# Performance work log

Hardware: AMD Instinct MI355X
Metric: run time of the kernel (lower is better)

Reference implementation:

```python
import jax, jax.numpy as jnp
import numpy as np

N_NODES = 50000
N_EDGES = 640000
IN_FEATS = 512
HID = 128
OUT_FEATS = 128
N_GRAPHS = 256


def setup_inputs() -> dict:
    key = jax.random.key(0)
    ks = jax.random.split(key, 7)
    x = jax.random.normal(ks[0], (N_NODES, IN_FEATS), dtype=jnp.float32)
    edge_index = jax.random.randint(ks[1], (2, N_EDGES), 0, N_NODES, dtype=jnp.int32)
    batch = jnp.sort(jax.random.randint(ks[2], (N_NODES,), 0, N_GRAPHS, dtype=jnp.int32))
    W1 = jax.random.normal(ks[3], (IN_FEATS, HID), dtype=jnp.float32) * (1.0 / np.sqrt(IN_FEATS))
    b1 = jnp.zeros((HID,), jnp.float32)
    W2 = jax.random.normal(ks[4], (HID, OUT_FEATS), dtype=jnp.float32) * (1.0 / np.sqrt(HID))
    b2 = jnp.zeros((OUT_FEATS,), jnp.float32)
    return {"x": x, "W1": W1, "b1": b1, "W2": W2, "b2": b2,
            "edge_index": edge_index, "batch": batch}


def reference(x, W1, b1, W2, b2, edge_index, batch):
    N = x.shape[0]
    loop = jnp.arange(N, dtype=edge_index.dtype)
    # PyG GCNConv default: add self-loops, symmetric deg^-1/2 normalization
    row = jnp.concatenate([edge_index[0], loop])  # source
    col = jnp.concatenate([edge_index[1], loop])  # target
    deg = jax.ops.segment_sum(jnp.ones_like(col, x.dtype), col, num_segments=N)
    dinv = jnp.where(deg > 0, jax.lax.rsqrt(deg), 0.0)
    norm = dinv[row] * dinv[col]  # [E+N]

    def gcn_conv(h, W, b):
        h = h @ W  # linear transform first (PyG order)
        msg = h[row] * norm[:, None]  # gather + scale
        agg = jax.ops.segment_sum(msg, col, num_segments=N)  # scatter-add
        return agg + b

    h = jax.nn.relu(gcn_conv(x, W1, b1))  # dropout is identity in eval mode
    h = gcn_conv(h, W2, b2)
    hs = jax.ops.segment_sum(h, batch, num_segments=N_GRAPHS)  # global_add_pool
    return hs, h
```

## Files before the change

kernel.cpp:

```cpp
#include <hip/hip_runtime.h>
#include <hip/hip_bf16.h>

#define N_NODES  50000
#define N_EDGES  640000
#define IN_FEATS 512
#define HID      128
#define OUT_FEATS 128
#define N_GRAPHS 256

#define SCAN_CHUNK 1024
#define SCAN_BLOCKS ((N_NODES + SCAN_CHUNK - 1) / SCAN_CHUNK)

typedef __attribute__((ext_vector_type(8))) short short8;
typedef __attribute__((ext_vector_type(4))) float f32x4;

__device__ __forceinline__ float bf2f(unsigned u16) {
    return __uint_as_float(u16 << 16);
}
__device__ __forceinline__ unsigned short f2bf(float f) {
    __hip_bfloat16 h = __float2bfloat16(f);
    return *(unsigned short*)&h;
}


#define PREP_BLOCKS 840

__global__ __launch_bounds__(256) void k_prep(const float* __restrict__ W1,
                                              const float* __restrict__ W2,
                                              const int* __restrict__ batch,
                                              unsigned short* __restrict__ wt1,
                                              unsigned short* __restrict__ wt2,
                                              int* __restrict__ cnt,
                                              int* __restrict__ gstart,
                                              float* __restrict__ hs) {
    int b = blockIdx.x;
    int t = threadIdx.x;
    if (b < 196) {
        int i = b * 256 + t;
        if (i < N_NODES) {
            int bt = batch[i];
            int bp = (i == 0) ? -1 : batch[i - 1];
            for (int g = bp + 1; g <= bt; ++g) gstart[g] = i;
            if (i == N_NODES - 1)
                for (int g = bt + 1; g <= N_GRAPHS; ++g) gstart[g] = N_NODES;
        }
    } else if (b < 392) {
        int i = (b - 196) * 256 + t;
        if (i < N_NODES) cnt[i] = 0;
    } else if (b < 648) {
        int idx = (b - 392) * 256 + t;
        int n = idx & 127, k = idx >> 7;
        wt1[(size_t)n * IN_FEATS + k] = f2bf(W1[(size_t)k * 128 + n]);
    } else if (b < 712) {
        int idx = (b - 648) * 256 + t;
        int n = idx & 127, k = idx >> 7;
        wt2[(size_t)n * HID + k] = f2bf(W2[(size_t)k * 128 + n]);
    } else {
        int idx = (b - 712) * 256 + t;
        hs[idx] = 0.f;
    }
}


__global__ void k_count(const int* __restrict__ col, int* __restrict__ cnt) {
    int e = blockIdx.x * blockDim.x + threadIdx.x;
    if (e < N_EDGES) atomicAdd(&cnt[col[e]], 1);
}

__global__ __launch_bounds__(256) void k_scan_a(const int* __restrict__ cnt,
                                                int* __restrict__ offs,
                                                int* __restrict__ bsum) {
    __shared__ int sums[256];
    int t = threadIdx.x;
    int base = blockIdx.x * SCAN_CHUNK + t * 4;
    int c0 = 0, c1 = 0, c2 = 0, c3 = 0;
    if (base + 3 < N_NODES) {
        int4 v = *(const int4*)(cnt + base);
        c0 = v.x; c1 = v.y; c2 = v.z; c3 = v.w;
    } else {
        if (base + 0 < N_NODES) c0 = cnt[base + 0];
        if (base + 1 < N_NODES) c1 = cnt[base + 1];
        if (base + 2 < N_NODES) c2 = cnt[base + 2];
    }
    int ts = c0 + c1 + c2 + c3;
    sums[t] = ts;
    __syncthreads();
#pragma unroll
    for (int off = 1; off < 256; off <<= 1) {
        int add = (t >= off) ? sums[t - off] : 0;
        __syncthreads();
        sums[t] += add;
        __syncthreads();
    }
    int ex = sums[t] - ts;
    if (base + 3 < N_NODES) {
        int4 o;
        o.x = ex; o.y = ex + c0; o.z = ex + c0 + c1; o.w = ex + c0 + c1 + c2;
        *(int4*)(offs + base) = o;
    } else {
        if (base + 0 < N_NODES) offs[base + 0] = ex;
        if (base + 1 < N_NODES) offs[base + 1] = ex + c0;
        if (base + 2 < N_NODES) offs[base + 2] = ex + c0 + c1;
    }
    if (t == 255) bsum[blockIdx.x] = sums[255];
}

__global__ __launch_bounds__(256) void k_scan_c(const int* __restrict__ cnt,
                                                const int* __restrict__ bsum,
                                                int* __restrict__ offs,
                                                int* __restrict__ cursor,
                                                float* __restrict__ dinv) {
    __shared__ int sb[64];
    int t = threadIdx.x;
    int b = blockIdx.x;
    if (t < 64) sb[t] = (t < SCAN_BLOCKS) ? bsum[t] : 0;
    __syncthreads();
#pragma unroll
    for (int off = 1; off < 64; off <<= 1) {
        int add = 0;
        if (t < 64 && t >= off) add = sb[t - off];
        __syncthreads();
        if (t < 64) sb[t] += add;
        __syncthreads();
    }
    int add = (b == 0) ? 0 : sb[b - 1];
    int base = b * SCAN_CHUNK + t * 4;
    if (base + 3 < N_NODES) {
        int4 o = *(const int4*)(offs + base);
        o.x += add; o.y += add; o.z += add; o.w += add;
        *(int4*)(offs + base) = o;
        *(int4*)(cursor + base) = o;
        int4 c = *(const int4*)(cnt + base);
        float4 d;
        d.x = rsqrtf((float)c.x + 1.0f);
        d.y = rsqrtf((float)c.y + 1.0f);
        d.z = rsqrtf((float)c.z + 1.0f);
        d.w = rsqrtf((float)c.w + 1.0f);
        *(float4*)(dinv + base) = d;
    } else {
#pragma unroll
        for (int j = 0; j < 4; ++j) {
            int i = base + j;
            if (i < N_NODES) {
                int o = offs[i] + add;
                offs[i] = o; cursor[i] = o;
                dinv[i] = rsqrtf((float)cnt[i] + 1.0f);
            }
        }
    }
    if (b == 0 && t == 0) offs[N_NODES] = N_EDGES;
}

__global__ void k_fill(const int* __restrict__ row, const int* __restrict__ col,
                       int* __restrict__ cursor, int* __restrict__ srcIdx) {
    int e = blockIdx.x * blockDim.x + threadIdx.x;
    if (e < N_EDGES) {
        int c = col[e];
        int p = atomicAdd(&cursor[c], 1);
        srcIdx[p] = row[e];
    }
}


template <int K>
__global__ __launch_bounds__(256) void k_gemm_mfma_f32a(const float* __restrict__ A,
                                                        const unsigned short* __restrict__ Bt,
                                                        unsigned short* __restrict__ Cb, int M) {
    __shared__ unsigned short As[4][64][8];
    __shared__ unsigned short Bs[4][128][8];
    int tid = threadIdx.x;
    int wave = tid >> 6;
    int lane = tid & 63;
    int quad = lane >> 4;
    int l15 = lane & 15;
    int m0 = blockIdx.x * 64;

    f32x4 acc[8];
#pragma unroll
    for (int nt = 0; nt < 8; ++nt) acc[nt] = (f32x4){0.f, 0.f, 0.f, 0.f};

    int gm_a = m0 + lane; if (gm_a >= M) gm_a = M - 1;
    const float* ap_base = A + (size_t)gm_a * K + wave * 8;

    for (int k0 = 0; k0 < K; k0 += 32) {
        {
            const float* ap = ap_base + k0;
            float4 v0 = *(const float4*)ap;
            float4 v1 = *(const float4*)(ap + 4);
            float f[8] = {v0.x, v0.y, v0.z, v0.w, v1.x, v1.y, v1.z, v1.w};
            short8 pk;
#pragma unroll
            for (int j = 0; j < 8; ++j) pk[j] = (short)f2bf(f[j]);
            *(short8*)&As[wave][lane][0] = pk;
        }
#pragma unroll
        for (int i = 0; i < 2; ++i) {
            int slot = tid + i * 256;
            int bkq = slot >> 7;
            int n = slot & 127;
            *(short8*)&Bs[bkq][n][0] = *(const short8*)(Bt + (size_t)n * K + k0 + bkq * 8);
        }
        __syncthreads();
        short8 a = *(short8*)&As[quad][wave * 16 + l15][0];
#pragma unroll
        for (int nt = 0; nt < 8; ++nt) {
            short8 b = *(short8*)&Bs[quad][nt * 16 + l15][0];
            acc[nt] = __builtin_amdgcn_mfma_f32_16x16x32_bf16(a, b, acc[nt], 0, 0, 0);
        }
        __syncthreads();
    }
    int row_base = m0 + wave * 16 + quad * 4;
#pragma unroll
    for (int nt = 0; nt < 8; ++nt) {
#pragma unroll
        for (int r2 = 0; r2 < 4; ++r2) {
            int gm = row_base + r2;
            if (gm < M) Cb[(size_t)gm * 128 + nt * 16 + l15] = f2bf(acc[nt][r2]);
        }
    }
}


template <int K>
__global__ __launch_bounds__(256) void k_gemm_mfma_bf16a(const unsigned short* __restrict__ A,
                                                         const unsigned short* __restrict__ Bt,
                                                         unsigned short* __restrict__ Cb, int M) {
    __shared__ unsigned short As[4][64][8];
    __shared__ unsigned short Bs[4][128][8];
    int tid = threadIdx.x;
    int wave = tid >> 6;
    int lane = tid & 63;
    int quad = lane >> 4;
    int l15 = lane & 15;
    int m0 = blockIdx.x * 64;

    f32x4 acc[8];
#pragma unroll
    for (int nt = 0; nt < 8; ++nt) acc[nt] = (f32x4){0.f, 0.f, 0.f, 0.f};

    int gm_a = m0 + lane; if (gm_a >= M) gm_a = M - 1;
    const unsigned short* ap_base = A + (size_t)gm_a * K + wave * 8;

    for (int k0 = 0; k0 < K; k0 += 32) {
        *(short8*)&As[wave][lane][0] = *(const short8*)(ap_base + k0);
#pragma unroll
        for (int i = 0; i < 2; ++i) {
            int slot = tid + i * 256;
            int bkq = slot >> 7;
            int n = slot & 127;
            *(short8*)&Bs[bkq][n][0] = *(const short8*)(Bt + (size_t)n * K + k0 + bkq * 8);
        }
        __syncthreads();
        short8 a = *(short8*)&As[quad][wave * 16 + l15][0];
#pragma unroll
        for (int nt = 0; nt < 8; ++nt) {
            short8 b = *(short8*)&Bs[quad][nt * 16 + l15][0];
            acc[nt] = __builtin_amdgcn_mfma_f32_16x16x32_bf16(a, b, acc[nt], 0, 0, 0);
        }
        __syncthreads();
    }
    int row_base = m0 + wave * 16 + quad * 4;
#pragma unroll
    for (int nt = 0; nt < 8; ++nt) {
#pragma unroll
        for (int r2 = 0; r2 < 4; ++r2) {
            int gm = row_base + r2;
            if (gm < M) Cb[(size_t)gm * 128 + nt * 16 + l15] = f2bf(acc[nt][r2]);
        }
    }
}


template <int RELU, int OUTBF>
__global__ __launch_bounds__(128) void k_agg(const unsigned* __restrict__ t,
                                             const int* __restrict__ offs,
                                             const int* __restrict__ srcIdx,
                                             const float* __restrict__ dinv,
                                             const float* __restrict__ bias,
                                             void* __restrict__ out_) {
    int wave = threadIdx.x >> 6;
    int lane = threadIdx.x & 63;
    int i = blockIdx.x * 2 + wave;
    float di = dinv[i];
    unsigned self = t[(size_t)i * 64 + lane];
    float s0 = bf2f(self & 0xffffu) * di;
    float s1 = bf2f(self >> 16) * di;
    int lo = offs[i], hi = offs[i + 1];
    int e = lo;
    for (; e + 8 <= hi; e += 8) {
        int idx[8];
#pragma unroll
        for (int j = 0; j < 8; ++j) idx[j] = srcIdx[e + j];
        unsigned v[8];
#pragma unroll
        for (int j = 0; j < 8; ++j) v[j] = t[(size_t)idx[j] * 64 + lane];
        float d[8];
#pragma unroll
        for (int j = 0; j < 8; ++j) d[j] = dinv[idx[j]];
#pragma unroll
        for (int j = 0; j < 8; ++j) {
            s0 = fmaf(bf2f(v[j] & 0xffffu), d[j], s0);
            s1 = fmaf(bf2f(v[j] >> 16), d[j], s1);
        }
    }
    for (; e < hi; ++e) {
        int sn = srcIdx[e];
        unsigned vv = t[(size_t)sn * 64 + lane];
        float dd = dinv[sn];
        s0 = fmaf(bf2f(vv & 0xffffu), dd, s0);
        s1 = fmaf(bf2f(vv >> 16), dd, s1);
    }
    float2 bb = *(const float2*)(bias + lane * 2);
    float r0 = s0 * di + bb.x;
    float r1 = s1 * di + bb.y;
    if (RELU) { r0 = fmaxf(r0, 0.f); r1 = fmaxf(r1, 0.f); }
    if (OUTBF) {
        unsigned o = (unsigned)f2bf(r0) | ((unsigned)f2bf(r1) << 16);
        ((unsigned*)out_)[(size_t)i * 64 + lane] = o;
    } else {
        *(float2*)((float*)out_ + (size_t)i * 128 + lane * 2) = make_float2(r0, r1);
    }
}


__global__ __launch_bounds__(128) void k_pool(const float* __restrict__ h,
                                              const int* __restrict__ gstart,
                                              float* __restrict__ hs) {
    int g = blockIdx.x >> 2;
    int c = blockIdx.x & 3;
    int f = threadIdx.x;
    int lo = gstart[g], hi = gstart[g + 1];
    int len = hi - lo;
    int chunk = (len + 3) >> 2;
    int r0 = lo + c * chunk;
    int r1 = r0 + chunk; if (r1 > hi) r1 = hi;
    if (r0 >= r1) return;
    float s = 0.f;
    for (int r = r0; r < r1; ++r) s += h[(size_t)r * 128 + f];
    atomicAdd(&hs[(size_t)g * 128 + f], s);
}


extern "C" void kernel_launch(void* const* d_in, const int* in_sizes, int n_in,
                              void* d_out, int out_size, void* d_ws, size_t ws_size,
                              hipStream_t stream) {
    const float* x  = (const float*)d_in[0];
    const float* W1 = (const float*)d_in[1];
    const float* b1 = (const float*)d_in[2];
    const float* W2 = (const float*)d_in[3];
    const float* b2 = (const float*)d_in[4];
    const int*   ei = (const int*)d_in[5];
    const int*   batch = (const int*)d_in[6];
    const int* row = ei;
    const int* col = ei + N_EDGES;

    float* out_hs = (float*)d_out;
    float* out_h  = (float*)d_out + N_GRAPHS * OUT_FEATS;

    char* ws = (char*)d_ws;
    unsigned short* tb   = (unsigned short*)ws;
    unsigned short* h1b  = (unsigned short*)(ws + 12800000);
    unsigned short* tb2  = (unsigned short*)(ws + 25600000);
    float* dinv = (float*)(ws + 38400000);
    int*   cnt    = (int*)(ws + 38600000);
    int*   offs   = (int*)(ws + 38800000);
    int*   cursor = (int*)(ws + 39000016);
    int*   srcIdx = (int*)(ws + 39200016);
    int*   gstart = (int*)(ws + 41760016);
    int*   bsum   = (int*)(ws + 41761056);
    unsigned short* wt1 = (unsigned short*)(ws + 41761472);
    unsigned short* wt2 = (unsigned short*)(ws + 41892544);

    const int TB = 256;
    k_prep<<<PREP_BLOCKS, 256, 0, stream>>>(W1, W2, batch, wt1, wt2, cnt, gstart, out_hs);
    k_count<<<(N_EDGES + TB - 1) / TB, TB, 0, stream>>>(col, cnt);
    k_scan_a<<<SCAN_BLOCKS, 256, 0, stream>>>(cnt, offs, bsum);
    k_scan_c<<<SCAN_BLOCKS, 256, 0, stream>>>(cnt, bsum, offs, cursor, dinv);
    k_fill<<<(N_EDGES + TB - 1) / TB, TB, 0, stream>>>(row, col, cursor, srcIdx);

    const int GB = (N_NODES + 63) / 64;
    k_gemm_mfma_f32a<IN_FEATS><<<GB, 256, 0, stream>>>(x, wt1, tb, N_NODES);
    k_agg<1, 1><<<N_NODES / 2, 128, 0, stream>>>((const unsigned*)tb, offs, srcIdx, dinv, b1, h1b);
    k_gemm_mfma_bf16a<HID><<<GB, 256, 0, stream>>>(h1b, wt2, tb2, N_NODES);
    k_agg<0, 0><<<N_NODES / 2, 128, 0, stream>>>((const unsigned*)tb2, offs, srcIdx, dinv, b2, out_h);
    k_pool<<<N_GRAPHS * 4, 128, 0, stream>>>(out_h, gstart, out_hs);
}
```

Measured before the change: 351.5 us.

## Reorder layer-2 to aggregate-then-transform, fuse pooling into GEMM, retile GEMM1

Layer 2 now aggregates the bf16 hidden features first (no bias) and then applies the linear transform, since aggregation commutes with the matmul. The second GEMM adds the bias, writes the fp32 output and does global-add pooling in its epilogue with run-length atomics keyed on the batch ids, which removes the separate pool kernel and the bf16 round trip of the transformed features. The first GEMM moves to 128x128 tiles with a 2x2 wave layout so each B tile is reused across more rows. The count and fill kernels each handle four edges per thread with vector loads. The changes shift where bf16 rounding happens and add atomic contention on the pooled output.

```diff
diff --git a/kernel.cpp b/kernel.cpp
--- a/kernel.cpp
+++ b/kernel.cpp
@@ -21,7 +21,6 @@
     __hip_bfloat16 h = __float2bfloat16(f);
     return *(unsigned short*)&h;
 }
-
 
 #define PREP_BLOCKS 840
 
@@ -63,8 +62,13 @@
 
 
 __global__ void k_count(const int* __restrict__ col, int* __restrict__ cnt) {
-    int e = blockIdx.x * blockDim.x + threadIdx.x;
-    if (e < N_EDGES) atomicAdd(&cnt[col[e]], 1);
+    int e4 = (blockIdx.x * blockDim.x + threadIdx.x) * 4;
+    if (e4 >= N_EDGES) return;
+    int4 c = *(const int4*)(col + e4);
+    atomicAdd(&cnt[c.x], 1);
+    atomicAdd(&cnt[c.y], 1);
+    atomicAdd(&cnt[c.z], 1);
+    atomicAdd(&cnt[c.w], 1);
 }
 
 __global__ __launch_bounds__(256) void k_scan_a(const int* __restrict__ cnt,
@@ -153,19 +157,103 @@
 
 __global__ void k_fill(const int* __restrict__ row, const int* __restrict__ col,
                        int* __restrict__ cursor, int* __restrict__ srcIdx) {
-    int e = blockIdx.x * blockDim.x + threadIdx.x;
-    if (e < N_EDGES) {
-        int c = col[e];
-        int p = atomicAdd(&cursor[c], 1);
-        srcIdx[p] = row[e];
-    }
+    int e4 = (blockIdx.x * blockDim.x + threadIdx.x) * 4;
+    if (e4 >= N_EDGES) return;
+    int4 r = *(const int4*)(row + e4);
+    int4 c = *(const int4*)(col + e4);
+    srcIdx[atomicAdd(&cursor[c.x], 1)] = r.x;
+    srcIdx[atomicAdd(&cursor[c.y], 1)] = r.y;
+    srcIdx[atomicAdd(&cursor[c.z], 1)] = r.z;
+    srcIdx[atomicAdd(&cursor[c.w], 1)] = r.w;
 }
 
 
 template <int K>
-__global__ __launch_bounds__(256) void k_gemm_mfma_f32a(const float* __restrict__ A,
-                                                        const unsigned short* __restrict__ Bt,
-                                                        unsigned short* __restrict__ Cb, int M) {
+__global__ __launch_bounds__(256) void k_gemm1(const float* __restrict__ A,
+                                               const unsigned short* __restrict__ Bt,
+                                               unsigned short* __restrict__ Cb, int M) {
+    __shared__ unsigned short As[4][128][8];
+    __shared__ unsigned short Bs[4][128][8];
+    int tid = threadIdx.x;
+    int wave = tid >> 6;
+    int lane = tid & 63;
+    int quad = lane >> 4;
+    int l15 = lane & 15;
+    int m0 = blockIdx.x * 128;
+    int mw = (wave >> 1) * 64;
+    int nw = (wave & 1) * 64;
+
+    f32x4 acc[4][4];
+#pragma unroll
+    for (int i = 0; i < 4; ++i)
+#pragma unroll
+        for (int j = 0; j < 4; ++j) acc[i][j] = (f32x4){0.f, 0.f, 0.f, 0.f};
+
+    int r0s = tid >> 2, kq0 = tid & 3;
+    int r1s = r0s + 64;
+    int gm0 = m0 + r0s; if (gm0 >= M) gm0 = M - 1;
+    int gm1 = m0 + r1s; if (gm1 >= M) gm1 = M - 1;
+    const float* ap0 = A + (size_t)gm0 * K + kq0 * 8;
+    const float* ap1 = A + (size_t)gm1 * K + kq0 * 8;
+
+    for (int k0 = 0; k0 < K; k0 += 32) {
+        {
+            float4 v0 = *(const float4*)(ap0 + k0);
+            float4 v1 = *(const float4*)(ap0 + k0 + 4);
+            float f[8] = {v0.x, v0.y, v0.z, v0.w, v1.x, v1.y, v1.z, v1.w};
+            short8 pk;
+#pragma unroll
+            for (int j = 0; j < 8; ++j) pk[j] = (short)f2bf(f[j]);
+            *(short8*)&As[kq0][r0s][0] = pk;
+            v0 = *(const float4*)(ap1 + k0);
+            v1 = *(const float4*)(ap1 + k0 + 4);
+            float g[8] = {v0.x, v0.y, v0.z, v0.w, v1.x, v1.y, v1.z, v1.w};
+#pragma unroll
+            for (int j = 0; j < 8; ++j) pk[j] = (short)f2bf(g[j]);
+            *(short8*)&As[kq0][r1s][0] = pk;
+        }
+#pragma unroll
+        for (int i = 0; i < 2; ++i) {
+            int slot = tid + i * 256;
+            int n = slot >> 2, kq = slot & 3;
+            *(short8*)&Bs[kq][n][0] = *(const short8*)(Bt + (size_t)n * K + k0 + kq * 8);
+        }
+        __syncthreads();
+        short8 af[4], bfr[4];
+#pragma unroll
+        for (int i = 0; i < 4; ++i) af[i] = *(short8*)&As[quad][mw + i * 16 + l15][0];
+#pragma unroll
+        for (int j = 0; j < 4; ++j) bfr[j] = *(short8*)&Bs[quad][nw + j * 16 + l15][0];
+#pragma unroll
+        for (int i = 0; i < 4; ++i)
+#pragma unroll
+            for (int j = 0; j < 4; ++j)
+                acc[i][j] = __builtin_amdgcn_mfma_f32_16x16x32_bf16(af[i], bfr[j], acc[i][j], 0, 0, 0);
+        __syncthreads();
+    }
+#pragma unroll
+    for (int i = 0; i < 4; ++i) {
+        int rb = m0 + mw + i * 16 + quad * 4;
+#pragma unroll
+        for (int j = 0; j < 4; ++j) {
+            int colb = nw + j * 16 + l15;
+#pragma unroll
+            for (int r2 = 0; r2 < 4; ++r2) {
+                int gm = rb + r2;
+                if (gm < M) Cb[(size_t)gm * 128 + colb] = f2bf(acc[i][j][r2]);
+            }
+        }
+    }
+}
+
+
+__global__ __launch_bounds__(256) void k_gemm2_pool(const unsigned short* __restrict__ G,
+                                                    const unsigned short* __restrict__ Bt,
+                                                    const float* __restrict__ bias,
+                                                    const int* __restrict__ batch,
+                                                    float* __restrict__ out,
+                                                    float* __restrict__ hs, int M) {
+    const int K = HID;
     __shared__ unsigned short As[4][64][8];
     __shared__ unsigned short Bs[4][128][8];
     int tid = threadIdx.x;
@@ -180,19 +268,10 @@
     for (int nt = 0; nt < 8; ++nt) acc[nt] = (f32x4){0.f, 0.f, 0.f, 0.f};
 
     int gm_a = m0 + lane; if (gm_a >= M) gm_a = M - 1;
-    const float* ap_base = A + (size_t)gm_a * K + wave * 8;
+    const unsigned short* ap_base = G + (size_t)gm_a * K + wave * 8;
 
     for (int k0 = 0; k0 < K; k0 += 32) {
-        {
-            const float* ap = ap_base + k0;
-            float4 v0 = *(const float4*)ap;
-            float4 v1 = *(const float4*)(ap + 4);
-            float f[8] = {v0.x, v0.y, v0.z, v0.w, v1.x, v1.y, v1.z, v1.w};
-            short8 pk;
-#pragma unroll
-            for (int j = 0; j < 8; ++j) pk[j] = (short)f2bf(f[j]);
-            *(short8*)&As[wave][lane][0] = pk;
-        }
+        *(short8*)&As[wave][lane][0] = *(const short8*)(ap_base + k0);
 #pragma unroll
         for (int i = 0; i < 2; ++i) {
             int slot = tid + i * 256;
@@ -209,64 +288,32 @@
         }
         __syncthreads();
     }
-    int row_base = m0 + wave * 16 + quad * 4;
+    int rb = m0 + wave * 16 + quad * 4;
+    int g_[4];
+#pragma unroll
+    for (int r2 = 0; r2 < 4; ++r2)
+        g_[r2] = (rb + r2 < M) ? batch[rb + r2] : -1;
 #pragma unroll
     for (int nt = 0; nt < 8; ++nt) {
+        int colb = nt * 16 + l15;
+        float bcol = bias[colb];
+        float v[4];
 #pragma unroll
         for (int r2 = 0; r2 < 4; ++r2) {
-            int gm = row_base + r2;
-            if (gm < M) Cb[(size_t)gm * 128 + nt * 16 + l15] = f2bf(acc[nt][r2]);
-        }
-    }
-}
-
-
-template <int K>
-__global__ __launch_bounds__(256) void k_gemm_mfma_bf16a(const unsigned short* __restrict__ A,
-                                                         const unsigned short* __restrict__ Bt,
-                                                         unsigned short* __restrict__ Cb, int M) {
-    __shared__ unsigned short As[4][64][8];
-    __shared__ unsigned short Bs[4][128][8];
-    int tid = threadIdx.x;
-    int wave = tid >> 6;
-    int lane = tid & 63;
-    int quad = lane >> 4;
-    int l15 = lane & 15;
-    int m0 = blockIdx.x * 64;
-
-    f32x4 acc[8];
-#pragma unroll
-    for (int nt = 0; nt < 8; ++nt) acc[nt] = (f32x4){0.f, 0.f, 0.f, 0.f};
-
-    int gm_a = m0 + lane; if (gm_a >= M) gm_a = M - 1;
-    const unsigned short* ap_base = A + (size_t)gm_a * K + wave * 8;
-
-    for (int k0 = 0; k0 < K; k0 += 32) {
-        *(short8*)&As[wave][lane][0] = *(const short8*)(ap_base + k0);
-#pragma unroll
-        for (int i = 0; i < 2; ++i) {
-            int slot = tid + i * 256;
-            int bkq = slot >> 7;
-            int n = slot & 127;
-            *(short8*)&Bs[bkq][n][0] = *(const short8*)(Bt + (size_t)n * K + k0 + bkq * 8);
-        }
-        __syncthreads();
-        short8 a = *(short8*)&As[quad][wave * 16 + l15][0];
-#pragma unroll
-        for (int nt = 0; nt < 8; ++nt) {
-            short8 b = *(short8*)&Bs[quad][nt * 16 + l15][0];
-            acc[nt] = __builtin_amdgcn_mfma_f32_16x16x32_bf16(a, b, acc[nt], 0, 0, 0);
-        }
-        __syncthreads();
-    }
-    int row_base = m0 + wave * 16 + quad * 4;
-#pragma unroll
-    for (int nt = 0; nt < 8; ++nt) {
-#pragma unroll
-        for (int r2 = 0; r2 < 4; ++r2) {
-            int gm = row_base + r2;
-            if (gm < M) Cb[(size_t)gm * 128 + nt * 16 + l15] = f2bf(acc[nt][r2]);
-        }
+            v[r2] = acc[nt][r2] + bcol;
+            if (rb + r2 < M) out[(size_t)(rb + r2) * 128 + colb] = v[r2];
+        }
+        float run = v[0];
+        int gcur = g_[0];
+#pragma unroll
+        for (int r2 = 1; r2 < 4; ++r2) {
+            if (g_[r2] == gcur) run += v[r2];
+            else {
+                if (gcur >= 0) atomicAdd(&hs[(size_t)gcur * 128 + colb], run);
+                gcur = g_[r2]; run = v[r2];
+            }
+        }
+        if (gcur >= 0) atomicAdd(&hs[(size_t)gcur * 128 + colb], run);
     }
 }
 
@@ -310,9 +357,12 @@
         s0 = fmaf(bf2f(vv & 0xffffu), dd, s0);
         s1 = fmaf(bf2f(vv >> 16), dd, s1);
     }
-    float2 bb = *(const float2*)(bias + lane * 2);
-    float r0 = s0 * di + bb.x;
-    float r1 = s1 * di + bb.y;
+    float r0 = s0 * di;
+    float r1 = s1 * di;
+    if (bias) {
+        float2 bb = *(const float2*)(bias + lane * 2);
+        r0 += bb.x; r1 += bb.y;
+    }
     if (RELU) { r0 = fmaxf(r0, 0.f); r1 = fmaxf(r1, 0.f); }
     if (OUTBF) {
         unsigned o = (unsigned)f2bf(r0) | ((unsigned)f2bf(r1) << 16);
@@ -320,24 +370,6 @@
     } else {
         *(float2*)((float*)out_ + (size_t)i * 128 + lane * 2) = make_float2(r0, r1);
     }
-}
-
-
-__global__ __launch_bounds__(128) void k_pool(const float* __restrict__ h,
-                                              const int* __restrict__ gstart,
-                                              float* __restrict__ hs) {
-    int g = blockIdx.x >> 2;
-    int c = blockIdx.x & 3;
-    int f = threadIdx.x;
-    int lo = gstart[g], hi = gstart[g + 1];
-    int len = hi - lo;
-    int chunk = (len + 3) >> 2;
-    int r0 = lo + c * chunk;
-    int r1 = r0 + chunk; if (r1 > hi) r1 = hi;
-    if (r0 >= r1) return;
-    float s = 0.f;
-    for (int r = r0; r < r1; ++r) s += h[(size_t)r * 128 + f];
-    atomicAdd(&hs[(size_t)g * 128 + f], s);
 }
 
 
@@ -360,7 +392,7 @@
     char* ws = (char*)d_ws;
     unsigned short* tb   = (unsigned short*)ws;
     unsigned short* h1b  = (unsigned short*)(ws + 12800000);
-    unsigned short* tb2  = (unsigned short*)(ws + 25600000);
+    unsigned short* gb   = (unsigned short*)(ws + 25600000);
     float* dinv = (float*)(ws + 38400000);
     int*   cnt    = (int*)(ws + 38600000);
     int*   offs   = (int*)(ws + 38800000);
@@ -373,15 +405,13 @@
 
     const int TB = 256;
     k_prep<<<PREP_BLOCKS, 256, 0, stream>>>(W1, W2, batch, wt1, wt2, cnt, gstart, out_hs);
-    k_count<<<(N_EDGES + TB - 1) / TB, TB, 0, stream>>>(col, cnt);
+    k_count<<<(N_EDGES / 4 + TB - 1) / TB, TB, 0, stream>>>(col, cnt);
     k_scan_a<<<SCAN_BLOCKS, 256, 0, stream>>>(cnt, offs, bsum);
     k_scan_c<<<SCAN_BLOCKS, 256, 0, stream>>>(cnt, bsum, offs, cursor, dinv);
-    k_fill<<<(N_EDGES + TB - 1) / TB, TB, 0, stream>>>(row, col, cursor, srcIdx);
-
-    const int GB = (N_NODES + 63) / 64;
-    k_gemm_mfma_f32a<IN_FEATS><<<GB, 256, 0, stream>>>(x, wt1, tb, N_NODES);
+    k_fill<<<(N_EDGES / 4 + TB - 1) / TB, TB, 0, stream>>>(row, col, cursor, srcIdx);
+
+    k_gemm1<IN_FEATS><<<(N_NODES + 127) / 128, 256, 0, stream>>>(x, wt1, tb, N_NODES);
     k_agg<1, 1><<<N_NODES / 2, 128, 0, stream>>>((const unsigned*)tb, offs, srcIdx, dinv, b1, h1b);
-    k_gemm_mfma_bf16a<HID><<<GB, 256, 0, stream>>>(h1b, wt2, tb2, N_NODES);
-    k_agg<0, 0><<<N_NODES / 2, 128, 0, stream>>>((const unsigned*)tb2, offs, srcIdx, dinv, b2, out_h);
-    k_pool<<<N_GRAPHS * 4, 128, 0, stream>>>(out_h, gstart, out_hs);
-}
+    k_agg<0, 1><<<N_NODES / 2, 128, 0, stream>>>((const unsigned*)h1b, offs, srcIdx, dinv, nullptr, gb);
+    k_gemm2_pool<<<(N_NODES + 63) / 64, 256, 0, stream>>>(gb, wt2, b2, batch, out_h, out_hs, N_NODES);
+}
```

Measured after the change: 345.6 us. Within noise of the previous version (-1.7%).
